# Performance work log

Measured on AMD Instinct MI355X. Metric: run time of the kernel, lower is better.

## Reference

```python
import jax, jax.numpy as jnp
import numpy as np

EPS = 1e-9
NEG = -99.0


def setup_inputs() -> dict:
    key = jax.random.key(0)
    k1, k2 = jax.random.split(key)
    N, D, LEN_PRD = 8192, 512, 4096
    embeddings = jax.random.normal(k1, (N, D), dtype=jnp.float32)
    W = jax.random.randint(k2, (N, N), 0, 2, dtype=jnp.int32)
    return {"embeddings": embeddings, "W": W, "len_prd": LEN_PRD, "head": 1}


def reference(embeddings, W, len_prd, head):
    # mask = -99 * (1 - W_block)
    Wb = (W[:len_prd, len_prd:] if head == 1 else W).astype(jnp.float32)
    mask = NEG * (1.0 - Wb)

    # row-normalize embeddings with eps clamp on norms
    norms = jnp.linalg.norm(embeddings, axis=1, keepdims=True)
    norms = jnp.where(norms <= EPS, EPS, norms)
    ne = embeddings / norms

    # cosine similarity; when head==1 only the [:len_prd, len_prd:] block is
    # kept, so compute just that block (same math as full matmul + slice)
    if head == 1:
        sim = ne[:len_prd] @ ne[len_prd:].T  # [len_prd, N-len_prd]
    else:
        sim = ne @ ne.T

    masked = sim + mask

    # output_matrix = clamp(relu(masked), max=1)
    output_matrix = jnp.minimum(jnp.maximum(masked, 0.0), 1.0)

    # half_normalized = 1 / (1 - masked); row-sum normalize with eps clamp
    half = 1.0 / (1.0 - masked)
    row_sum = jnp.sum(half, axis=1, keepdims=True)
    row_sum = jnp.where(row_sum <= EPS, EPS, row_sum)
    normed = half / row_sum

    # supple flag: 1 if no positive entry in the masked row, else 0;
    # zero out flagged rows and append the flag as an extra column
    supple = jnp.where(jnp.any(masked > 0.0, axis=1), 0.0, 1.0)  # [x_len]
    processed = jnp.where(supple[:, None] == 1.0, 0.0, normed)
    extended = jnp.concatenate([processed, supple[:, None]], axis=1)

    return (output_matrix, extended)
```

## Files before the change

### kernel.cpp

```cpp
#include <hip/hip_runtime.h>
#include <hip/hip_bf16.h>
#include <stdint.h>

#define NROW 8192
#define DIM  512
#define LP   4096
#define NB   4096
#define EXTW 4097
#define NEGC (-99.0f)
#define EPSF 1e-9f

typedef __attribute__((ext_vector_type(8))) __bf16 bf16x8;
typedef __attribute__((ext_vector_type(4))) float f32x4;

__global__ __launch_bounds__(256) void k_norm(const float* __restrict__ emb,
                                              __hip_bfloat16* __restrict__ ne) {
    const int row = blockIdx.x;
    const int t = threadIdx.x;
    const float* rp = emb + (size_t)row * DIM;
    float2 v = *(const float2*)(rp + t * 2);
    float s = v.x * v.x + v.y * v.y;
    #pragma unroll
    for (int off = 32; off; off >>= 1) s += __shfl_down(s, off);
    __shared__ float wsum[4];
    const int wid = t >> 6, lane = t & 63;
    if (lane == 0) wsum[wid] = s;
    __syncthreads();
    float tot = wsum[0] + wsum[1] + wsum[2] + wsum[3];
    float nrm = sqrtf(tot);
    nrm = (nrm <= EPSF) ? EPSF : nrm;
    const float inv = 1.0f / nrm;
    __hip_bfloat162 pk;
    pk.x = __float2bfloat16(v.x * inv);
    pk.y = __float2bfloat16(v.y * inv);
    *(__hip_bfloat162*)(ne + (size_t)row * DIM + t * 2) = pk;
}

#define BM 128
#define BN 128
#define BK 64
#define SIMLD 132

#define GLOAD_LDS(gp, lp) __builtin_amdgcn_global_load_lds(                     \
    (const __attribute__((address_space(1))) uint32_t*)(gp),                    \
    (__attribute__((address_space(3))) uint32_t*)(lp), 16, 0, 0)

__global__ __launch_bounds__(256) void k_gemm(const __hip_bfloat16* __restrict__ ne,
                                              const int* __restrict__ W,
                                              float* __restrict__ out0,
                                              float* __restrict__ ext) {
    __shared__ __align__(16) char smem[32768];
    __bf16* As = (__bf16*)smem;
    __bf16* Bs = (__bf16*)(smem + 16384);
    float*  Sim = (float*)smem;

    const int bid = blockIdx.x;
    const int wg = (bid & 7) * 128 + (bid >> 3);
    const int tileR = wg >> 5, tileC = wg & 31;

    const int tid = threadIdx.x;
    const int lane = tid & 63, wid = tid >> 6;
    const int wr = wid >> 1, wc = wid & 1;
    const int r16 = lane & 15, kg = lane >> 4;

    const __bf16* A = (const __bf16*)ne + (size_t)(tileR * BM) * DIM;
    const __bf16* B = (const __bf16*)ne + (size_t)(LP + tileC * BN) * DIM;

    const int srow = lane >> 3;
    const int scol = (lane & 7) * 8;

    f32x4 acc[4][4] = {};

    for (int kt = 0; kt < 8; ++kt) {
        const int k0 = kt * BK;
        #pragma unroll
        for (int i = 0; i < 4; ++i) {
            const int seg = wid * 4 + i;
            const int r = seg * 8 + srow;
            GLOAD_LDS(A + (size_t)r * DIM + k0 + scol, As + seg * 512);
            GLOAD_LDS(B + (size_t)r * DIM + k0 + scol, Bs + seg * 512);
        }
        __syncthreads();
        #pragma unroll
        for (int kk = 0; kk < 2; ++kk) {
            bf16x8 af[4], bfr[4];
            #pragma unroll
            for (int m = 0; m < 4; ++m)
                af[m] = *(const bf16x8*)(As + (wr * 64 + m * 16 + r16) * 64 + kk * 32 + kg * 8);
            #pragma unroll
            for (int n = 0; n < 4; ++n)
                bfr[n] = *(const bf16x8*)(Bs + (wc * 64 + n * 16 + r16) * 64 + kk * 32 + kg * 8);
            #pragma unroll
            for (int m = 0; m < 4; ++m)
                #pragma unroll
                for (int n = 0; n < 4; ++n)
                    acc[m][n] = __builtin_amdgcn_mfma_f32_16x16x32_bf16(af[m], bfr[n], acc[m][n], 0, 0, 0);
        }
        __syncthreads();
    }

    const int gr_base = tileR * BM;
    const int gc_base = tileC * BN;
    #pragma unroll
    for (int m = 0; m < 4; ++m) {
        __syncthreads();
        #pragma unroll
        for (int n = 0; n < 4; ++n)
            #pragma unroll
            for (int j = 0; j < 4; ++j)
                Sim[(wr * 16 + kg * 4 + j) * SIMLD + wc * 64 + n * 16 + r16] = acc[m][n][j];
        __syncthreads();
        #pragma unroll
        for (int p = 0; p < 4; ++p) {
            const int lr = p * 8 + (tid >> 5);
            const int cc = (tid & 31) * 4;
            const int gr = gr_base + ((lr >> 4) << 6) + m * 16 + (lr & 15);
            const int gc = gc_base + cc;
            const float4 s4 = *(const float4*)(Sim + lr * SIMLD + cc);
            const int4 w4 = *(const int4*)(W + (size_t)gr * NROW + LP + gc);
            const float m0 = w4.x ? s4.x : (s4.x + NEGC);
            const float m1 = w4.y ? s4.y : (s4.y + NEGC);
            const float m2 = w4.z ? s4.z : (s4.z + NEGC);
            const float m3 = w4.w ? s4.w : (s4.w + NEGC);
            float4 o;
            o.x = fminf(fmaxf(m0, 0.0f), 1.0f);
            o.y = fminf(fmaxf(m1, 0.0f), 1.0f);
            o.z = fminf(fmaxf(m2, 0.0f), 1.0f);
            o.w = fminf(fmaxf(m3, 0.0f), 1.0f);
            *(float4*)(out0 + (size_t)gr * NB + gc) = o;
            float* ex = ext + (size_t)gr * EXTW + gc;
            ex[0] = 1.0f / (1.0f - m0);
            ex[1] = 1.0f / (1.0f - m1);
            ex[2] = 1.0f / (1.0f - m2);
            ex[3] = 1.0f / (1.0f - m3);
        }
    }
}

__global__ __launch_bounds__(256) void k_final(float* __restrict__ ext) {
    const int row = blockIdx.x;
    float* rp = ext + (size_t)row * EXTW;
    const int t = threadIdx.x;
    float v[16];
    float s = 0.0f;
    int any = 0;
    #pragma unroll
    for (int i = 0; i < 16; ++i) {
        v[i] = rp[t + i * 256];
        s += v[i];
        any |= (v[i] > 1.0f) ? 1 : 0;
    }
    #pragma unroll
    for (int off = 32; off; off >>= 1) {
        s += __shfl_down(s, off);
        any |= __shfl_down(any, off);
    }
    __shared__ float ss[4];
    __shared__ int sa[4];
    const int wid = t >> 6, lane = t & 63;
    if (lane == 0) { ss[wid] = s; sa[wid] = any; }
    __syncthreads();
    float tot = ss[0] + ss[1] + ss[2] + ss[3];
    const int anyt = sa[0] | sa[1] | sa[2] | sa[3];
    tot = (tot <= EPSF) ? EPSF : tot;
    const float inv = anyt ? (1.0f / tot) : 0.0f;
    #pragma unroll
    for (int i = 0; i < 16; ++i) rp[t + i * 256] = v[i] * inv;
    if (t == 0) rp[NB] = anyt ? 0.0f : 1.0f;
}

extern "C" void kernel_launch(void* const* d_in, const int* in_sizes, int n_in,
                              void* d_out, int out_size, void* d_ws, size_t ws_size,
                              hipStream_t stream) {
    const float* emb = (const float*)d_in[0];
    const int* W = (const int*)d_in[1];

    float* out0 = (float*)d_out;
    float* ext = (float*)d_out + (size_t)LP * NB;
    __hip_bfloat16* ne = (__hip_bfloat16*)d_ws;

    k_norm<<<dim3(NROW), dim3(256), 0, stream>>>(emb, ne);
    k_gemm<<<dim3((LP / BM) * (NB / BN)), dim3(256), 0, stream>>>(ne, W, out0, ext);
    k_final<<<dim3(LP), dim3(256), 0, stream>>>(ext);
}
```

Before: 85.09 us.

## Prefetch W in GEMM epilogue and stage half values in aligned workspace

The GEMM epilogue now software-pipelines the W mask loads, fetching the next m-slice's int4 values into registers before the LDS write and read. It replaces __syncthreads with a custom barrier that waits only on LDS counters, so outstanding global loads can stay in flight. The 1/(1-masked) values are written as float4 into a workspace with a 4096-float row stride instead of scalar stores into the odd-stride (4097) output, and the final kernel reads them with float4 loads. This adds a separate 64MB workspace write and read plus extra registers for the prefetched W, and the final kernel's stores into the output are still scalar and unaligned.

```diff
diff --git a/kernel.cpp b/kernel.cpp
--- a/kernel.cpp
+++ b/kernel.cpp
@@ -12,6 +12,13 @@
 
 typedef __attribute__((ext_vector_type(8))) __bf16 bf16x8;
 typedef __attribute__((ext_vector_type(4))) float f32x4;
+
+#define LDS_BARRIER do {                                    \
+    __builtin_amdgcn_sched_barrier(0);                      \
+    asm volatile("s_waitcnt lgkmcnt(0)" ::: "memory");      \
+    __builtin_amdgcn_s_barrier();                           \
+    __builtin_amdgcn_sched_barrier(0);                      \
+} while (0)
 
 __global__ __launch_bounds__(256) void k_norm(const float* __restrict__ emb,
                                               __hip_bfloat16* __restrict__ ne) {
@@ -45,10 +52,10 @@
     (const __attribute__((address_space(1))) uint32_t*)(gp),                    \
     (__attribute__((address_space(3))) uint32_t*)(lp), 16, 0, 0)
 
-__global__ __launch_bounds__(256) void k_gemm(const __hip_bfloat16* __restrict__ ne,
-                                              const int* __restrict__ W,
-                                              float* __restrict__ out0,
-                                              float* __restrict__ ext) {
+__global__ __launch_bounds__(256, 4) void k_gemm(const __hip_bfloat16* __restrict__ ne,
+                                                 const int* __restrict__ W,
+                                                 float* __restrict__ out0,
+                                                 float* __restrict__ half_ws) {
     __shared__ __align__(16) char smem[32768];
     __bf16* As = (__bf16*)smem;
     __bf16* Bs = (__bf16*)(smem + 16384);
@@ -101,23 +108,37 @@
 
     const int gr_base = tileR * BM;
     const int gc_base = tileC * BN;
+    const int lr = (tid >> 5);
+    const int cc = (tid & 31) * 4;
+
+    int4 wreg[2][4];
+    auto LOADW = [&](int m, int4 (&wq)[4]) {
+        #pragma unroll
+        for (int p = 0; p < 4; ++p) {
+            const int r = p * 8 + lr;
+            const int gr = gr_base + ((r >> 4) << 6) + m * 16 + (r & 15);
+            wq[p] = *(const int4*)(W + (size_t)gr * NROW + LP + gc_base + cc);
+        }
+    };
+
+    LOADW(0, wreg[0]);
     #pragma unroll
     for (int m = 0; m < 4; ++m) {
-        __syncthreads();
+        LDS_BARRIER;
+        if (m < 3) LOADW(m + 1, wreg[(m + 1) & 1]);
         #pragma unroll
         for (int n = 0; n < 4; ++n)
             #pragma unroll
             for (int j = 0; j < 4; ++j)
                 Sim[(wr * 16 + kg * 4 + j) * SIMLD + wc * 64 + n * 16 + r16] = acc[m][n][j];
-        __syncthreads();
+        LDS_BARRIER;
         #pragma unroll
         for (int p = 0; p < 4; ++p) {
-            const int lr = p * 8 + (tid >> 5);
-            const int cc = (tid & 31) * 4;
-            const int gr = gr_base + ((lr >> 4) << 6) + m * 16 + (lr & 15);
+            const int r = p * 8 + lr;
+            const int gr = gr_base + ((r >> 4) << 6) + m * 16 + (r & 15);
             const int gc = gc_base + cc;
-            const float4 s4 = *(const float4*)(Sim + lr * SIMLD + cc);
-            const int4 w4 = *(const int4*)(W + (size_t)gr * NROW + LP + gc);
+            const float4 s4 = *(const float4*)(Sim + r * SIMLD + cc);
+            const int4 w4 = wreg[m & 1][p];
             const float m0 = w4.x ? s4.x : (s4.x + NEGC);
             const float m1 = w4.y ? s4.y : (s4.y + NEGC);
             const float m2 = w4.z ? s4.z : (s4.z + NEGC);
@@ -128,27 +149,30 @@
             o.z = fminf(fmaxf(m2, 0.0f), 1.0f);
             o.w = fminf(fmaxf(m3, 0.0f), 1.0f);
             *(float4*)(out0 + (size_t)gr * NB + gc) = o;
-            float* ex = ext + (size_t)gr * EXTW + gc;
-            ex[0] = 1.0f / (1.0f - m0);
-            ex[1] = 1.0f / (1.0f - m1);
-            ex[2] = 1.0f / (1.0f - m2);
-            ex[3] = 1.0f / (1.0f - m3);
-        }
-    }
-}
-
-__global__ __launch_bounds__(256) void k_final(float* __restrict__ ext) {
+            float4 h;
+            h.x = 1.0f / (1.0f - m0);
+            h.y = 1.0f / (1.0f - m1);
+            h.z = 1.0f / (1.0f - m2);
+            h.w = 1.0f / (1.0f - m3);
+            *(float4*)(half_ws + (size_t)gr * NB + gc) = h;
+        }
+    }
+}
+
+__global__ __launch_bounds__(256) void k_final(const float* __restrict__ half_ws,
+                                               float* __restrict__ ext) {
     const int row = blockIdx.x;
+    const float* hp = half_ws + (size_t)row * NB;
     float* rp = ext + (size_t)row * EXTW;
     const int t = threadIdx.x;
-    float v[16];
+    float4 v[4];
     float s = 0.0f;
     int any = 0;
     #pragma unroll
-    for (int i = 0; i < 16; ++i) {
-        v[i] = rp[t + i * 256];
-        s += v[i];
-        any |= (v[i] > 1.0f) ? 1 : 0;
+    for (int i = 0; i < 4; ++i) {
+        v[i] = *(const float4*)(hp + t * 4 + i * 1024);
+        s += (v[i].x + v[i].y) + (v[i].z + v[i].w);
+        any |= (v[i].x > 1.0f) | (v[i].y > 1.0f) | (v[i].z > 1.0f) | (v[i].w > 1.0f);
     }
     #pragma unroll
     for (int off = 32; off; off >>= 1) {
@@ -165,7 +189,13 @@
     tot = (tot <= EPSF) ? EPSF : tot;
     const float inv = anyt ? (1.0f / tot) : 0.0f;
     #pragma unroll
-    for (int i = 0; i < 16; ++i) rp[t + i * 256] = v[i] * inv;
+    for (int i = 0; i < 4; ++i) {
+        float* op = rp + t * 4 + i * 1024;
+        op[0] = v[i].x * inv;
+        op[1] = v[i].y * inv;
+        op[2] = v[i].z * inv;
+        op[3] = v[i].w * inv;
+    }
     if (t == 0) rp[NB] = anyt ? 0.0f : 1.0f;
 }
 
@@ -178,8 +208,9 @@
     float* out0 = (float*)d_out;
     float* ext = (float*)d_out + (size_t)LP * NB;
     __hip_bfloat16* ne = (__hip_bfloat16*)d_ws;
+    float* half_ws = (float*)((char*)d_ws + (size_t)16 * 1024 * 1024);
 
     k_norm<<<dim3(NROW), dim3(256), 0, stream>>>(emb, ne);
-    k_gemm<<<dim3((LP / BM) * (NB / BN)), dim3(256), 0, stream>>>(ne, W, out0, ext);
-    k_final<<<dim3(LP), dim3(256), 0, stream>>>(ext);
-}
+    k_gemm<<<dim3((LP / BM) * (NB / BN)), dim3(256), 0, stream>>>(ne, W, out0, half_ws);
+    k_final<<<dim3(LP), dim3(256), 0, stream>>>(half_ws, ext);
+}
```

After: 119.8 us. 40.8% more time.

## Store half matrix as bf16 scratch and compute row partial sums in GEMM epilogue

Applied to the files above, without the earlier changes.

The GEMM epilogue now writes the 1/(1-masked) values to a bf16 scratch buffer instead of fp32 into the output. It also reduces per-tile partial row sums and any-positive flags, which the final kernel combines before scaling and writing the fp32 output. This halves the intermediate write and read traffic and removes the full reduction pass in the final kernel. The cost is the precision of the half values, which are rounded to bf16 before normalization, plus extra shuffle reductions in the epilogue.

```diff
diff --git a/kernel.cpp b/kernel.cpp
--- a/kernel.cpp
+++ b/kernel.cpp
@@ -48,7 +48,9 @@
 __global__ __launch_bounds__(256) void k_gemm(const __hip_bfloat16* __restrict__ ne,
                                               const int* __restrict__ W,
                                               float* __restrict__ out0,
-                                              float* __restrict__ ext) {
+                                              __hip_bfloat16* __restrict__ half16,
+                                              float* __restrict__ psum,
+                                              int* __restrict__ pany) {
     __shared__ __align__(16) char smem[32768];
     __bf16* As = (__bf16*)smem;
     __bf16* Bs = (__bf16*)(smem + 16384);
@@ -101,6 +103,9 @@
 
     const int gr_base = tileR * BM;
     const int gc_base = tileC * BN;
+    const int lr = (tid >> 5);
+    const int cc = (tid & 31) * 4;
+
     #pragma unroll
     for (int m = 0; m < 4; ++m) {
         __syncthreads();
@@ -112,11 +117,10 @@
         __syncthreads();
         #pragma unroll
         for (int p = 0; p < 4; ++p) {
-            const int lr = p * 8 + (tid >> 5);
-            const int cc = (tid & 31) * 4;
-            const int gr = gr_base + ((lr >> 4) << 6) + m * 16 + (lr & 15);
+            const int r = p * 8 + lr;
+            const int gr = gr_base + ((r >> 4) << 6) + m * 16 + (r & 15);
             const int gc = gc_base + cc;
-            const float4 s4 = *(const float4*)(Sim + lr * SIMLD + cc);
+            const float4 s4 = *(const float4*)(Sim + r * SIMLD + cc);
             const int4 w4 = *(const int4*)(W + (size_t)gr * NROW + LP + gc);
             const float m0 = w4.x ? s4.x : (s4.x + NEGC);
             const float m1 = w4.y ? s4.y : (s4.y + NEGC);
@@ -128,45 +132,61 @@
             o.z = fminf(fmaxf(m2, 0.0f), 1.0f);
             o.w = fminf(fmaxf(m3, 0.0f), 1.0f);
             *(float4*)(out0 + (size_t)gr * NB + gc) = o;
-            float* ex = ext + (size_t)gr * EXTW + gc;
-            ex[0] = 1.0f / (1.0f - m0);
-            ex[1] = 1.0f / (1.0f - m1);
-            ex[2] = 1.0f / (1.0f - m2);
-            ex[3] = 1.0f / (1.0f - m3);
-        }
-    }
-}
-
-__global__ __launch_bounds__(256) void k_final(float* __restrict__ ext) {
+            const float h0 = 1.0f / (1.0f - m0);
+            const float h1 = 1.0f / (1.0f - m1);
+            const float h2 = 1.0f / (1.0f - m2);
+            const float h3 = 1.0f / (1.0f - m3);
+            __hip_bfloat16 hp[4] = {__float2bfloat16(h0), __float2bfloat16(h1),
+                                    __float2bfloat16(h2), __float2bfloat16(h3)};
+            *(ushort4*)(half16 + (size_t)gr * NB + gc) = *(const ushort4*)hp;
+            float ps = (h0 + h1) + (h2 + h3);
+            int pa = (m0 > 0.0f) | (m1 > 0.0f) | (m2 > 0.0f) | (m3 > 0.0f);
+            #pragma unroll
+            for (int off = 1; off < 32; off <<= 1) {
+                ps += __shfl_xor(ps, off);
+                pa |= __shfl_xor(pa, off);
+            }
+            if ((tid & 31) == 0) {
+                psum[(size_t)gr * 32 + tileC] = ps;
+                pany[(size_t)gr * 32 + tileC] = pa;
+            }
+        }
+    }
+}
+
+__global__ __launch_bounds__(256) void k_final(const __hip_bfloat16* __restrict__ half16,
+                                               const float* __restrict__ psum,
+                                               const int* __restrict__ pany,
+                                               float* __restrict__ ext) {
     const int row = blockIdx.x;
+    const int t = threadIdx.x;
+    __shared__ float sInv;
+    __shared__ int sAny;
+    if (t < 64) {
+        float s = (t < 32) ? psum[(size_t)row * 32 + t] : 0.0f;
+        int a = (t < 32) ? pany[(size_t)row * 32 + t] : 0;
+        #pragma unroll
+        for (int off = 16; off; off >>= 1) {
+            s += __shfl_xor(s, off);
+            a |= __shfl_xor(a, off);
+        }
+        if (t == 0) {
+            float tot = (s <= EPSF) ? EPSF : s;
+            sInv = a ? (1.0f / tot) : 0.0f;
+            sAny = a;
+        }
+    }
+    __syncthreads();
+    const float inv = sInv;
+    const uint16_t* hp = (const uint16_t*)(half16 + (size_t)row * NB);
     float* rp = ext + (size_t)row * EXTW;
-    const int t = threadIdx.x;
-    float v[16];
-    float s = 0.0f;
-    int any = 0;
     #pragma unroll
     for (int i = 0; i < 16; ++i) {
-        v[i] = rp[t + i * 256];
-        s += v[i];
-        any |= (v[i] > 1.0f) ? 1 : 0;
-    }
-    #pragma unroll
-    for (int off = 32; off; off >>= 1) {
-        s += __shfl_down(s, off);
-        any |= __shfl_down(any, off);
-    }
-    __shared__ float ss[4];
-    __shared__ int sa[4];
-    const int wid = t >> 6, lane = t & 63;
-    if (lane == 0) { ss[wid] = s; sa[wid] = any; }
-    __syncthreads();
-    float tot = ss[0] + ss[1] + ss[2] + ss[3];
-    const int anyt = sa[0] | sa[1] | sa[2] | sa[3];
-    tot = (tot <= EPSF) ? EPSF : tot;
-    const float inv = anyt ? (1.0f / tot) : 0.0f;
-    #pragma unroll
-    for (int i = 0; i < 16; ++i) rp[t + i * 256] = v[i] * inv;
-    if (t == 0) rp[NB] = anyt ? 0.0f : 1.0f;
+        const int c = t + i * 256;
+        const uint32_t u = (uint32_t)hp[c] << 16;
+        rp[c] = __uint_as_float(u) * inv;
+    }
+    if (t == 0) rp[NB] = sAny ? 0.0f : 1.0f;
 }
 
 extern "C" void kernel_launch(void* const* d_in, const int* in_sizes, int n_in,
@@ -178,8 +198,11 @@
     float* out0 = (float*)d_out;
     float* ext = (float*)d_out + (size_t)LP * NB;
     __hip_bfloat16* ne = (__hip_bfloat16*)d_ws;
+    __hip_bfloat16* half16 = (__hip_bfloat16*)((char*)d_ws + ((size_t)16 << 20));
+    float* psum = (float*)((char*)d_ws + ((size_t)48 << 20));
+    int*   pany = (int*)((char*)d_ws + ((size_t)49 << 20));
 
     k_norm<<<dim3(NROW), dim3(256), 0, stream>>>(emb, ne);
-    k_gemm<<<dim3((LP / BM) * (NB / BN)), dim3(256), 0, stream>>>(ne, W, out0, ext);
-    k_final<<<dim3(LP), dim3(256), 0, stream>>>(ext);
-}
+    k_gemm<<<dim3((LP / BM) * (NB / BN)), dim3(256), 0, stream>>>(ne, W, out0, half16, psum, pany);
+    k_final<<<dim3(LP), dim3(256), 0, stream>>>(half16, psum, pany, ext);
+}
```

After: 82.75 us. 2.7% less time.
